# Optimization experiments

Measured on AMD Instinct MI355X. Metric: run time of the kernel, lower is better.

## Reference

```python
import jax, jax.numpy as jnp
import numpy as np


def setup_inputs() -> dict:
    key = jax.random.key(0)
    ks = jax.random.split(key, 7)
    B, I, H = 16384, 1024, 1024
    s = 1.0 / np.sqrt(H)
    return {
        "x": jax.random.normal(ks[0], (B, I), jnp.float32),
        "h_prev": jax.random.normal(ks[1], (B, H), jnp.float32),
        "c_prev": jax.random.normal(ks[2], (B, H), jnp.float32),
        "Wx": jax.random.normal(ks[3], (4, H, I), jnp.float32) * s,  # gates z,i,f,o
        "bx": jax.random.normal(ks[4], (4, H), jnp.float32) * s,
        "Rh": jax.random.normal(ks[5], (4, H, H), jnp.float32) * s,
        "bh": jax.random.normal(ks[6], (4, H), jnp.float32) * s,
    }


def reference(x, h_prev, c_prev, Wx, bx, Rh, bh):
    # Fused: 2 batched GEMMs for all 4 gates, then one elementwise block.
    # gates_x[g] = x @ Wx[g].T + bx[g]  (g in z,i,f,o), same for Rh/h_prev.
    gx = jnp.einsum('bi,ghi->gbh', x, Wx) + bx[:, None, :]       # [4,B,H]
    gh = jnp.einsum('bh,gkh->gbk', h_prev, Rh) + bh[:, None, :]  # [4,B,H]
    pre = gx + gh
    z = jnp.tanh(pre[0])
    i = jax.nn.sigmoid(pre[1])
    f = jax.nn.sigmoid(pre[2])
    o = jax.nn.sigmoid(pre[3])
    c = f * c_prev + i * z
    h = o * jnp.tanh(c)
    return (h, c)
```

## Files before the change

kernel.cpp:

```cpp
#include <hip/hip_runtime.h>
#include <stdint.h>

typedef __bf16 bf16;
typedef __bf16 bf16x8 __attribute__((ext_vector_type(8)));
typedef float  f32x4  __attribute__((ext_vector_type(4)));
typedef float  fvec4  __attribute__((ext_vector_type(4)));

#define B_DIM 16384
#define H_DIM 1024
#define K_DIM 2048
#define NKT   32

__device__ __forceinline__ void g2l16(const void* g, void* l) {
    __builtin_amdgcn_global_load_lds(
        (const __attribute__((address_space(1))) void*)g,
        (__attribute__((address_space(3))) void*)l,
        16, 0, 0);
}

__device__ __forceinline__ float sigm_fast(float x) {
    x = fminf(fmaxf(x, -40.f), 40.f);
    float e = __builtin_amdgcn_exp2f(-1.4426950408889634f * x);
    return __builtin_amdgcn_rcpf(1.0f + e);
}
__device__ __forceinline__ float tanh_fast(float x) {
    x = fminf(fmaxf(x, -40.f), 40.f);
    float e = __builtin_amdgcn_exp2f(-2.8853900817779268f * x);
    return (1.0f - e) * __builtin_amdgcn_rcpf(1.0f + e);
}

__device__ __forceinline__ bf16x8 cvt8(const float* __restrict__ src) {
    fvec4 a = __builtin_nontemporal_load((const fvec4*)src);
    fvec4 b = __builtin_nontemporal_load((const fvec4*)(src + 4));
    bf16x8 o = { (bf16)a.x, (bf16)a.y, (bf16)a.z, (bf16)a.w,
                 (bf16)b.x, (bf16)b.y, (bf16)b.z, (bf16)b.w };
    return o;
}

__global__ __launch_bounds__(256) void cvt_all(const float* __restrict__ x,
                                               const float* __restrict__ h,
                                               const float* __restrict__ Wx,
                                               const float* __restrict__ Rh,
                                               const float* __restrict__ bx,
                                               const float* __restrict__ bh,
                                               bf16* __restrict__ U,
                                               bf16* __restrict__ W,
                                               float* __restrict__ bb) {
    int b = blockIdx.x;
    if (b < 16384) {
        const float* src0 = (b < 8192) ? x : h;
        int half = (b < 8192) ? 0 : 1024;
        int gid  = (b & 8191) * 256 + threadIdx.x;
        int row  = gid >> 7;
        int c    = gid & 127;
        bf16x8 o = cvt8(src0 + ((size_t)row << 10) + (c << 3));
        *(bf16x8*)(U + ((size_t)row << 11) + half + (c << 3)) = o;
    } else {
        int gid = (b - 16384) * 256 + threadIdx.x;
        if (gid < 524288) {
            int row = gid >> 7;
            int c   = gid & 127;
            bf16x8 o = cvt8(Wx + ((size_t)row << 10) + (c << 3));
            *(bf16x8*)(W + ((size_t)row << 11) + (c << 3)) = o;
        } else {
            int g2  = gid - 524288;
            int row = g2 >> 7;
            int c   = g2 & 127;
            bf16x8 o = cvt8(Rh + ((size_t)row << 10) + (c << 3));
            *(bf16x8*)(W + ((size_t)row << 11) + 1024 + (c << 3)) = o;
        }
        if (gid < 4096) bb[gid] = bx[gid] + bh[gid];
    }
}

__global__ __launch_bounds__(512, 2)
void lstm_fused(const bf16* __restrict__ U, const bf16* __restrict__ W,
                const float* __restrict__ bb, const float* __restrict__ cprev,
                float* __restrict__ out) {
    __shared__ __align__(16) bf16 As[2][256 * 64];
    __shared__ __align__(16) bf16 Bs[2][256 * 64];

    const int tid  = threadIdx.x;
    const int wave = tid >> 6;
    const int lane = tid & 63;
    const int quad = lane >> 4;
    const int lc   = lane & 15;
    const int wm   = wave >> 2;
    const int wn   = wave & 3;

    int bid   = blockIdx.x;
    int xcd   = bid & 7;
    int t     = bid >> 3;
    int h_idx = (xcd << 1) + (t >> 6);
    int m_idx = t & 63;
    const int m0 = m_idx << 8;
    const int h0 = h_idx << 6;

    uint32_t offA[2][2], offB[2][2];
    uint32_t lofs[2];
#pragma unroll
    for (int ld = 0; ld < 2; ++ld) {
        int slot  = (ld << 9) + tid;
        int row   = slot >> 3;
        int chunk = slot & 7;
        int colb  = (chunk ^ (row & 7)) << 4;
        lofs[ld]  = slot << 4;
#pragma unroll
        for (int hf = 0; hf < 2; ++hf) {
            int arow = m0 + (hf << 7) + row;
            offA[ld][hf] = ((uint32_t)arow << 12) + colb;
            int br   = (hf << 7) + row;
            int gate = (br >> 4) & 3;
            int hl   = ((br >> 6) << 4) + (br & 15);
            int wrow = (gate << 10) + h0 + hl;
            offB[ld][hf] = ((uint32_t)wrow << 12) + colb;
        }
    }
    const char* Ub = (const char*)U;
    const char* Wb = (const char*)W;
    char* AsB = (char*)As;
    char* BsB = (char*)Bs;

#define STG_A(hf, dbuf, ktt) do {                                              \
        g2l16(Ub + offA[0][hf] + ((ktt) << 7),                                 \
              AsB + ((dbuf) << 15) + ((hf) << 14) + lofs[0]);                  \
        g2l16(Ub + offA[1][hf] + ((ktt) << 7),                                 \
              AsB + ((dbuf) << 15) + ((hf) << 14) + lofs[1]);                  \
    } while (0)
#define STG_B(hf, dbuf, ktt) do {                                              \
        g2l16(Wb + offB[0][hf] + ((ktt) << 7),                                 \
              BsB + ((dbuf) << 15) + ((hf) << 14) + lofs[0]);                  \
        g2l16(Wb + offB[1][hf] + ((ktt) << 7),                                 \
              BsB + ((dbuf) << 15) + ((hf) << 14) + lofs[1]);                  \
    } while (0)

#define LDFRAG(BASEB, dbuf, row, ks)                                           \
    (*(const bf16x8*)((BASEB) + ((dbuf) << 15) + ((row) << 7) +                \
                      ((((((ks) << 2)) + quad) ^ (lc & 7)) << 4)))

#define MFMA_Q(MIBASE, NIBASE)                                                 \
    do {                                                                       \
        _Pragma("unroll")                                                      \
        for (int mi = 0; mi < 4; ++mi)                                         \
            _Pragma("unroll")                                                  \
            for (int ni = 0; ni < 2; ++ni)                                     \
                _Pragma("unroll")                                              \
                for (int ks = 0; ks < 2; ++ks)                                 \
                    acc[(MIBASE) + mi][(NIBASE) + ni] =                        \
                        __builtin_amdgcn_mfma_f32_16x16x32_bf16(               \
                            a_[mi][ks], b_[(NIBASE) + ni][ks],                 \
                            acc[(MIBASE) + mi][(NIBASE) + ni], 0, 0, 0);       \
    } while (0)

    f32x4 acc[8][4];
#pragma unroll
    for (int mi = 0; mi < 8; ++mi)
#pragma unroll
        for (int ni = 0; ni < 4; ++ni)
            acc[mi][ni] = (f32x4){0.f, 0.f, 0.f, 0.f};

    STG_B(0, 0, 0);
    STG_A(0, 0, 0);
    STG_A(1, 0, 0);
    STG_B(1, 0, 0);
    STG_B(0, 1, 1);
    STG_A(0, 1, 1);
    asm volatile("s_waitcnt vmcnt(4)" ::: "memory");
    __builtin_amdgcn_s_barrier();

    const int rA0 = (wm << 7) + lc;
    const int rB0 = (wn << 6) + lc;

    bf16x8 a_[4][2];
    bf16x8 b_[4][2];

#pragma clang loop unroll(disable)
    for (int kt = 0; kt < NKT; ++kt) {
        const int buf = kt & 1;

#pragma unroll
        for (int mi = 0; mi < 4; ++mi) {
            a_[mi][0] = LDFRAG(AsB, buf, rA0 + (mi << 4), 0);
            a_[mi][1] = LDFRAG(AsB, buf, rA0 + (mi << 4), 1);
        }
#pragma unroll
        for (int ni = 0; ni < 2; ++ni) {
            b_[ni][0] = LDFRAG(BsB, buf, rB0 + (ni << 4), 0);
            b_[ni][1] = LDFRAG(BsB, buf, rB0 + (ni << 4), 1);
        }
        if (kt < NKT - 1) STG_A(1, buf ^ 1, kt + 1);
        __builtin_amdgcn_s_barrier();
        asm volatile("s_waitcnt lgkmcnt(0)" ::: "memory");
        __builtin_amdgcn_s_setprio(1);
        MFMA_Q(0, 0);
        __builtin_amdgcn_s_setprio(0);
        __builtin_amdgcn_s_barrier();

#pragma unroll
        for (int ni = 2; ni < 4; ++ni) {
            b_[ni][0] = LDFRAG(BsB, buf, rB0 + (ni << 4), 0);
            b_[ni][1] = LDFRAG(BsB, buf, rB0 + (ni << 4), 1);
        }
        if (kt < NKT - 1) STG_B(1, buf ^ 1, kt + 1);
        __builtin_amdgcn_s_barrier();
        asm volatile("s_waitcnt lgkmcnt(0)" ::: "memory");
        __builtin_amdgcn_s_setprio(1);
        MFMA_Q(0, 2);
        __builtin_amdgcn_s_setprio(0);
        __builtin_amdgcn_s_barrier();

#pragma unroll
        for (int mi = 0; mi < 4; ++mi) {
            a_[mi][0] = LDFRAG(AsB, buf, rA0 + 64 + (mi << 4), 0);
            a_[mi][1] = LDFRAG(AsB, buf, rA0 + 64 + (mi << 4), 1);
        }
        if (kt < NKT - 2) STG_B(0, buf, kt + 2);
        __builtin_amdgcn_s_barrier();
        asm volatile("s_waitcnt lgkmcnt(0)" ::: "memory");
        __builtin_amdgcn_s_setprio(1);
        MFMA_Q(4, 0);
        __builtin_amdgcn_s_setprio(0);
        __builtin_amdgcn_s_barrier();

        if (kt < NKT - 2) STG_A(0, buf, kt + 2);
        __builtin_amdgcn_s_barrier();
        __builtin_amdgcn_s_setprio(1);
        MFMA_Q(4, 2);
        __builtin_amdgcn_s_setprio(0);
        if (kt < NKT - 2) {
            asm volatile("s_waitcnt vmcnt(4)" ::: "memory");
        } else if (kt == NKT - 2) {
            asm volatile("s_waitcnt vmcnt(0)" ::: "memory");
        }
        __builtin_amdgcn_s_barrier();
    }

    const int h = h0 + (wn << 4) + lc;
    float bias[4];
#pragma unroll
    for (int g = 0; g < 4; ++g) bias[g] = bb[(g << 10) + h];

    float* out_h = out;
    float* out_c = out + (size_t)B_DIM * H_DIM;
#pragma unroll
    for (int mi = 0; mi < 8; ++mi) {
#pragma unroll
        for (int r = 0; r < 4; ++r) {
            int brow  = m0 + (wm << 7) + (mi << 4) + (quad << 2) + r;
            size_t rb = (size_t)brow << 10;
            float zp = acc[mi][0][r] + bias[0];
            float ip = acc[mi][1][r] + bias[1];
            float fp = acc[mi][2][r] + bias[2];
            float op = acc[mi][3][r] + bias[3];
            float zz = tanh_fast(zp);
            float ii = sigm_fast(ip);
            float ff = sigm_fast(fp);
            float oo = sigm_fast(op);
            float cp = cprev[rb + h];
            float cn = ff * cp + ii * zz;
            float hn = oo * tanh_fast(cn);
            out_h[rb + h] = hn;
            out_c[rb + h] = cn;
        }
    }
}

extern "C" void kernel_launch(void* const* d_in, const int* in_sizes, int n_in,
                              void* d_out, int out_size, void* d_ws, size_t ws_size,
                              hipStream_t stream) {
    const float* x  = (const float*)d_in[0];
    const float* hp = (const float*)d_in[1];
    const float* cp = (const float*)d_in[2];
    const float* Wx = (const float*)d_in[3];
    const float* bx = (const float*)d_in[4];
    const float* Rh = (const float*)d_in[5];
    const float* bh = (const float*)d_in[6];

    bf16*  U  = (bf16*)d_ws;
    bf16*  W  = (bf16*)((char*)d_ws + (size_t)67108864);
    float* bb = (float*)((char*)d_ws + (size_t)67108864 + 16777216);

    cvt_all<<<20480, 256, 0, stream>>>(x, hp, Wx, Rh, bx, bh, U, W, bb);
    lstm_fused<<<1024, 512, 0, stream>>>(U, W, bb, cp, (float*)d_out);
}
```

Baseline: 535.3 us.

## Halve GEMM main-loop barriers and restructure fp32-to-bf16 conversion kernel

The GEMM main loop goes from eight workgroup barriers per k-tile to four. It drops the explicit lgkmcnt waits and loads all B fragments in the first phase, so LDS reads and MFMAs can overlap with less synchronisation. The conversion kernel now has each thread convert four rows with 16-byte loads and 8-byte stores, uses half as many blocks and drops the nontemporal hints. Removing barriers relies on the compiler's inserted waits for correctness, which risks LDS read/write hazards between the async global-to-LDS stages and the fragment reads.

```diff
diff --git a/kernel.cpp b/kernel.cpp
--- a/kernel.cpp
+++ b/kernel.cpp
@@ -2,6 +2,7 @@
 #include <stdint.h>
 
 typedef __bf16 bf16;
+typedef __bf16 bf16x4 __attribute__((ext_vector_type(4)));
 typedef __bf16 bf16x8 __attribute__((ext_vector_type(8)));
 typedef float  f32x4  __attribute__((ext_vector_type(4)));
 typedef float  fvec4  __attribute__((ext_vector_type(4)));
@@ -27,14 +28,6 @@
     x = fminf(fmaxf(x, -40.f), 40.f);
     float e = __builtin_amdgcn_exp2f(-2.8853900817779268f * x);
     return (1.0f - e) * __builtin_amdgcn_rcpf(1.0f + e);
-}
-
-__device__ __forceinline__ bf16x8 cvt8(const float* __restrict__ src) {
-    fvec4 a = __builtin_nontemporal_load((const fvec4*)src);
-    fvec4 b = __builtin_nontemporal_load((const fvec4*)(src + 4));
-    bf16x8 o = { (bf16)a.x, (bf16)a.y, (bf16)a.z, (bf16)a.w,
-                 (bf16)b.x, (bf16)b.y, (bf16)b.z, (bf16)b.w };
-    return o;
 }
 
 __global__ __launch_bounds__(256) void cvt_all(const float* __restrict__ x,
@@ -46,30 +39,33 @@
                                                bf16* __restrict__ U,
                                                bf16* __restrict__ W,
                                                float* __restrict__ bb) {
-    int b = blockIdx.x;
-    if (b < 16384) {
-        const float* src0 = (b < 8192) ? x : h;
-        int half = (b < 8192) ? 0 : 1024;
-        int gid  = (b & 8191) * 256 + threadIdx.x;
-        int row  = gid >> 7;
-        int c    = gid & 127;
-        bf16x8 o = cvt8(src0 + ((size_t)row << 10) + (c << 3));
-        *(bf16x8*)(U + ((size_t)row << 11) + half + (c << 3)) = o;
+    const int b   = blockIdx.x;
+    const int tid = threadIdx.x;
+    const float* src;
+    bf16* dst;
+    int half, blk;
+    if (b < 8192) {
+        src  = (b < 4096) ? x : h;
+        half = (b < 4096) ? 0 : 1024;
+        dst  = U;
+        blk  = b & 4095;
     } else {
-        int gid = (b - 16384) * 256 + threadIdx.x;
-        if (gid < 524288) {
-            int row = gid >> 7;
-            int c   = gid & 127;
-            bf16x8 o = cvt8(Wx + ((size_t)row << 10) + (c << 3));
-            *(bf16x8*)(W + ((size_t)row << 11) + (c << 3)) = o;
-        } else {
-            int g2  = gid - 524288;
-            int row = g2 >> 7;
-            int c   = g2 & 127;
-            bf16x8 o = cvt8(Rh + ((size_t)row << 10) + (c << 3));
-            *(bf16x8*)(W + ((size_t)row << 11) + 1024 + (c << 3)) = o;
-        }
-        if (gid < 4096) bb[gid] = bx[gid] + bh[gid];
+        int wb = b - 8192;
+        src  = (wb < 1024) ? Wx : Rh;
+        half = (wb < 1024) ? 0 : 1024;
+        dst  = W;
+        blk  = wb & 1023;
+    }
+    const float* s0 = src + (((size_t)blk << 2) << 10) + (tid << 2);
+    bf16*        d0 = dst + (((size_t)blk << 2) << 11) + half + (tid << 2);
+#pragma unroll
+    for (int u = 0; u < 4; ++u) {
+        fvec4 v = *(const fvec4*)(s0 + (u << 10));
+        bf16x4 o = {(bf16)v.x, (bf16)v.y, (bf16)v.z, (bf16)v.w};
+        *(bf16x4*)(d0 + (u << 11)) = o;
+    }
+    if (b == 0) {
+        for (int i = tid; i < 4096; i += 256) bb[i] = bx[i] + bh[i];
     }
 }
 
@@ -166,7 +162,6 @@
     STG_B(0, 1, 1);
     STG_A(0, 1, 1);
     asm volatile("s_waitcnt vmcnt(4)" ::: "memory");
-    __builtin_amdgcn_s_barrier();
 
     const int rA0 = (wm << 7) + lc;
     const int rB0 = (wn << 6) + lc;
@@ -178,52 +173,41 @@
     for (int kt = 0; kt < NKT; ++kt) {
         const int buf = kt & 1;
 
+        __builtin_amdgcn_s_barrier();
+        if (kt < NKT - 1) STG_A(1, buf ^ 1, kt + 1);
 #pragma unroll
         for (int mi = 0; mi < 4; ++mi) {
             a_[mi][0] = LDFRAG(AsB, buf, rA0 + (mi << 4), 0);
             a_[mi][1] = LDFRAG(AsB, buf, rA0 + (mi << 4), 1);
         }
 #pragma unroll
-        for (int ni = 0; ni < 2; ++ni) {
+        for (int ni = 0; ni < 4; ++ni) {
             b_[ni][0] = LDFRAG(BsB, buf, rB0 + (ni << 4), 0);
             b_[ni][1] = LDFRAG(BsB, buf, rB0 + (ni << 4), 1);
         }
-        if (kt < NKT - 1) STG_A(1, buf ^ 1, kt + 1);
-        __builtin_amdgcn_s_barrier();
-        asm volatile("s_waitcnt lgkmcnt(0)" ::: "memory");
         __builtin_amdgcn_s_setprio(1);
         MFMA_Q(0, 0);
         __builtin_amdgcn_s_setprio(0);
-        __builtin_amdgcn_s_barrier();
-
-#pragma unroll
-        for (int ni = 2; ni < 4; ++ni) {
-            b_[ni][0] = LDFRAG(BsB, buf, rB0 + (ni << 4), 0);
-            b_[ni][1] = LDFRAG(BsB, buf, rB0 + (ni << 4), 1);
-        }
+
+        __builtin_amdgcn_s_barrier();
         if (kt < NKT - 1) STG_B(1, buf ^ 1, kt + 1);
-        __builtin_amdgcn_s_barrier();
-        asm volatile("s_waitcnt lgkmcnt(0)" ::: "memory");
         __builtin_amdgcn_s_setprio(1);
         MFMA_Q(0, 2);
         __builtin_amdgcn_s_setprio(0);
-        __builtin_amdgcn_s_barrier();
-
 #pragma unroll
         for (int mi = 0; mi < 4; ++mi) {
             a_[mi][0] = LDFRAG(AsB, buf, rA0 + 64 + (mi << 4), 0);
             a_[mi][1] = LDFRAG(AsB, buf, rA0 + 64 + (mi << 4), 1);
         }
+
+        __builtin_amdgcn_s_barrier();
         if (kt < NKT - 2) STG_B(0, buf, kt + 2);
-        __builtin_amdgcn_s_barrier();
-        asm volatile("s_waitcnt lgkmcnt(0)" ::: "memory");
         __builtin_amdgcn_s_setprio(1);
         MFMA_Q(4, 0);
         __builtin_amdgcn_s_setprio(0);
-        __builtin_amdgcn_s_barrier();
-
+
+        __builtin_amdgcn_s_barrier();
         if (kt < NKT - 2) STG_A(0, buf, kt + 2);
-        __builtin_amdgcn_s_barrier();
         __builtin_amdgcn_s_setprio(1);
         MFMA_Q(4, 2);
         __builtin_amdgcn_s_setprio(0);
@@ -232,7 +216,6 @@
         } else if (kt == NKT - 2) {
             asm volatile("s_waitcnt vmcnt(0)" ::: "memory");
         }
-        __builtin_amdgcn_s_barrier();
     }
 
     const int h = h0 + (wn << 4) + lc;
@@ -280,6 +263,6 @@
     bf16*  W  = (bf16*)((char*)d_ws + (size_t)67108864);
     float* bb = (float*)((char*)d_ws + (size_t)67108864 + 16777216);
 
-    cvt_all<<<20480, 256, 0, stream>>>(x, hp, Wx, Rh, bx, bh, U, W, bb);
+    cvt_all<<<10240, 256, 0, stream>>>(x, hp, Wx, Rh, bx, bh, U, W, bb);
     lstm_fused<<<1024, 512, 0, stream>>>(U, W, bb, cp, (float*)d_out);
 }
```

Result: slower. 550.7 us (+2.9%).
